# Performance work log

Hardware: AMD Instinct MI355X
Metric: run time of the kernel (lower is better)

The kernel has to match this reference:

```python
import jax, jax.numpy as jnp
import numpy as np

N, E, B = 100000, 1600000, 64
IN, HID, OUT, ED = 64, 128, 128, 2
K, ALPHA = 16, 0.1
LN_EPS = 1e-5


def setup_inputs() -> dict:
    key = jax.random.key(0)
    ks = jax.random.split(key, 24)
    def gl(k, shape, fan_in):
        return jax.random.uniform(k, shape, jnp.float32, -1.0, 1.0) / np.sqrt(fan_in)
    inp = {
        "x": jax.random.normal(ks[0], (N, IN), jnp.float32),
        "edge_index": jax.random.randint(ks[1], (2, E), 0, N, jnp.int64),
        "batch": jnp.sort(jax.random.randint(ks[2], (N,), 0, B, jnp.int64)),
        "edge_attr": jax.random.normal(ks[3], (E, ED), jnp.float32),
        # conv1: edge lin (ED->IN) + mlp (IN->HID->HID)
        "We1": gl(ks[4], (ED, IN), ED), "be1": jnp.zeros((IN,)),
        "W1a": gl(ks[5], (IN, HID), IN), "b1a": jnp.zeros((HID,)),
        "W1b": gl(ks[6], (HID, HID), HID), "b1b": jnp.zeros((HID,)),
        "g1": jnp.ones((HID,)), "bn1": jnp.zeros((HID,)),
        # conv2: edge lin (ED->HID) + mlp (HID->OUT->OUT)
        "We2": gl(ks[7], (ED, HID), ED), "be2": jnp.zeros((HID,)),
        "W2a": gl(ks[8], (HID, OUT), HID), "b2a": jnp.zeros((OUT,)),
        "W2b": gl(ks[9], (OUT, OUT), OUT), "b2b": jnp.zeros((OUT,)),
        "g2": jnp.ones((OUT,)), "bn2": jnp.zeros((OUT,)),
        # gate nn (OUT -> OUT//2 -> 1)
        "Wg1": gl(ks[10], (OUT, OUT // 2), OUT), "bg1": jnp.zeros((OUT // 2,)),
        "Wg2": gl(ks[11], (OUT // 2, 1), OUT // 2), "bg2": jnp.zeros((1,)),
    }
    return inp


def _gelu(x):
    return jax.nn.gelu(x, approximate=False)


def _layernorm(x, g, b):
    mu = jnp.mean(x, axis=-1, keepdims=True)
    var = jnp.mean(jnp.square(x - mu), axis=-1, keepdims=True)
    return (x - mu) * jax.lax.rsqrt(var + LN_EPS) * g + b


def _gine(x, src, dst, edge_attr, We, be, W1, b1, W2, b2):
    # message: ReLU(x_j + lin(edge_attr)), aggregated by sum at dst; eps=0
    m = jax.nn.relu(x[src] + edge_attr @ We + be)          # [E, d]
    agg = jax.ops.segment_sum(m, dst, num_segments=N)      # [N, d]
    h = x + agg
    return _gelu(h @ W1 + b1) @ W2 + b2


def _appnp(x, src, dst):
    # gcn_norm with self-loops: deg_i = 1 + in-degree
    deg = jax.ops.segment_sum(jnp.ones((E,), x.dtype), dst, num_segments=N) + 1.0
    dis = jax.lax.rsqrt(deg)
    w = dis[src] * dis[dst]            # [E]
    selfw = 1.0 / deg                  # [N]
    def step(i, h):
        prop = jax.ops.segment_sum(w[:, None] * h[src], dst, num_segments=N) \
               + selfw[:, None] * h
        return (1.0 - ALPHA) * prop + ALPHA * x
    return jax.lax.fori_loop(0, K, step, x)


def reference(x, edge_index, batch, edge_attr,
              We1, be1, W1a, b1a, W1b, b1b, g1, bn1,
              We2, be2, W2a, b2a, W2b, b2b, g2, bn2,
              Wg1, bg1, Wg2, bg2):
    src, dst = edge_index[0], edge_index[1]
    h = _gine(x, src, dst, edge_attr, We1, be1, W1a, b1a, W1b, b1b)
    h = _layernorm(_gelu(h), g1, bn1)
    # dropout is identity in eval
    h = _gine(h, src, dst, edge_attr, We2, be2, W2a, b2a, W2b, b2b)
    h = _layernorm(h, g2, bn2)
    h = _appnp(h, src, dst)
    # attentional aggregation: per-graph softmax over gate scores
    gate = (_gelu(h @ Wg1 + bg1) @ Wg2 + bg2)[:, 0]        # [N]
    m = jax.ops.segment_max(gate, batch, num_segments=B)    # [B]
    e = jnp.exp(gate - m[batch])
    s = jax.ops.segment_sum(e, batch, num_segments=B)
    a = e / s[batch]
    g = jax.ops.segment_sum(a[:, None] * h, batch, num_segments=B)  # [B, OUT]
    return h, g
```

## Files before the change

kernel.cpp:

```cpp
#include <hip/hip_runtime.h>
#include <math.h>

#define N_NODES 100000
#define N_EDGES 1600000
#define N_B 64
#define D_IN 64
#define D_HID 128
#define D_OUT 128
#define K_ITER 16
#define LN_EPS 1e-5f

#define BSH 9
#define NBUCK 196
#define NBUCK_PAD 200
#define BSPLIT 4
#define CHUNK 2048

typedef short s8v __attribute__((ext_vector_type(8)));
typedef float f4v __attribute__((ext_vector_type(4)));

__device__ __forceinline__ float gelu_f(float x) {
    return 0.5f * x * (1.0f + erff(0.70710678118654752440f * x));
}

__device__ __forceinline__ float ubx(unsigned u) { return __uint_as_float(u << 16); }
__device__ __forceinline__ float uby(unsigned u) { return __uint_as_float(u & 0xffff0000u); }

__device__ __forceinline__ unsigned short bf_rne(float x) {
    unsigned u = __float_as_uint(x);
    u += 0x7fffu + ((u >> 16) & 1u);
    return (unsigned short)(u >> 16);
}
__device__ __forceinline__ float bf_f(unsigned short s) {
    return __uint_as_float(((unsigned)s) << 16);
}
__device__ __forceinline__ unsigned pack_bf2(float a, float b) {
    return (unsigned)bf_rne(a) | (((unsigned)bf_rne(b)) << 16);
}


__global__ __launch_bounds__(256) void hist_kernel(const int* __restrict__ dst, int* __restrict__ counts) {
    int e = blockIdx.x * 256 + threadIdx.x;
    if (e < N_EDGES) atomicAdd(&counts[dst[e]], 1);
}

__global__ __launch_bounds__(256) void deg_kernel(const int* __restrict__ counts,
                                                  float* __restrict__ dis, float* __restrict__ selfw,
                                                  float* __restrict__ rsq) {
    int i = blockIdx.x * 256 + threadIdx.x;
    if (i < N_NODES) {
        float d = (float)(counts[i] + 1);
        dis[i] = 1.0f / sqrtf(d);
        selfw[i] = 1.0f / d;
        rsq[i] = sqrtf(d);
    }
}

__global__ __launch_bounds__(1024) void scan1(const int* __restrict__ counts, int* __restrict__ rp,
                                              int* __restrict__ bsum) {
    __shared__ int tmp[1024];
    int t = threadIdx.x;
    int idx = blockIdx.x * 1024 + t;
    int v = (idx < N_NODES) ? counts[idx] : 0;
    tmp[t] = v;
    __syncthreads();
    for (int o = 1; o < 1024; o <<= 1) {
        int add = (t >= o) ? tmp[t - o] : 0;
        __syncthreads();
        tmp[t] += add;
        __syncthreads();
    }
    if (idx < N_NODES) rp[idx] = tmp[t] - v;
    if (t == 1023) bsum[blockIdx.x] = tmp[t];
}

__global__ void scan2(int* bsum, int nb) {
    if (threadIdx.x == 0 && blockIdx.x == 0) {
        int acc = 0;
        for (int i = 0; i < nb; i++) { int v = bsum[i]; bsum[i] = acc; acc += v; }
    }
}

__global__ __launch_bounds__(1024) void scan3(int* __restrict__ rp, const int* __restrict__ bsum,
                                              int* __restrict__ cursor) {
    int t = threadIdx.x;
    int idx = blockIdx.x * 1024 + t;
    if (idx < N_NODES) {
        int v = rp[idx] + bsum[blockIdx.x];
        rp[idx] = v;
        cursor[idx] = v;
    }
    if (idx == 0) rp[N_NODES] = N_EDGES;
}

__global__ void binit(const int* __restrict__ rp, int* __restrict__ bcursor) {
    int b = threadIdx.x;
    if (b < NBUCK) bcursor[b] = rp[b << BSH];
}

__global__ __launch_bounds__(256) void bin_kernel(const int* __restrict__ src, const int* __restrict__ dst,
                                                  const float* __restrict__ ea,
                                                  int* __restrict__ bcursor, int4* __restrict__ tmp) {
    __shared__ int hist[NBUCK];
    __shared__ int loff[NBUCK];
    __shared__ int gbase[NBUCK];
    __shared__ int total_s;
    __shared__ int4 stage[CHUNK];
    int tid = threadIdx.x;
    int base = blockIdx.x * CHUNK;
    for (int t = tid; t < NBUCK; t += 256) hist[t] = 0;
    __syncthreads();
    int4 rec[8];
    int bk[8], rk[8];
    bool val[8];
    #pragma unroll
    for (int k = 0; k < 8; k++) {
        int e = base + k * 256 + tid;
        val[k] = (e < N_EDGES);
        if (val[k]) {
            int s = src[e], d = dst[e];
            float2 e2 = ((const float2*)ea)[e];
            rec[k].x = s;
            rec[k].y = __float_as_int(e2.x);
            rec[k].z = __float_as_int(e2.y);
            rec[k].w = d;
            bk[k] = d >> BSH;
            rk[k] = atomicAdd(&hist[bk[k]], 1);
        }
    }
    __syncthreads();
    if (tid == 0) {
        int acc = 0;
        for (int b = 0; b < NBUCK; b++) { loff[b] = acc; acc += hist[b]; }
        total_s = acc;
    }
    __syncthreads();
    if (tid < NBUCK && hist[tid] > 0) gbase[tid] = atomicAdd(&bcursor[tid], hist[tid]);
    __syncthreads();
    #pragma unroll
    for (int k = 0; k < 8; k++)
        if (val[k]) stage[loff[bk[k]] + rk[k]] = rec[k];
    __syncthreads();
    int total = total_s;
    for (int s = tid; s < total; s += 256) {
        int lo = 0, hi = NBUCK - 1;
        while (lo < hi) {
            int mid = (lo + hi + 1) >> 1;
            if (loff[mid] <= s) lo = mid; else hi = mid - 1;
        }
        tmp[gbase[lo] + (s - loff[lo])] = stage[s];
    }
}

__global__ __launch_bounds__(256) void scatter2_kernel(const int4* __restrict__ tmp, const int* __restrict__ rp,
                                                       int* __restrict__ cursor, int4* __restrict__ edata) {
    int b = blockIdx.x % NBUCK_PAD;
    int slice = blockIdx.x / NBUCK_PAD;
    if (b >= NBUCK) return;
    int lo = rp[b << BSH];
    int nend = (b + 1) << BSH;
    if (nend > N_NODES) nend = N_NODES;
    int hi = rp[nend];
    for (int i = lo + slice * 256 + threadIdx.x; i < hi; i += BSPLIT * 256) {
        int4 r = tmp[i];
        int pos = atomicAdd(&cursor[r.w], 1);
        edata[pos] = r;
    }
}

__global__ __launch_bounds__(256) void split_kernel(const int4* __restrict__ edata, int* __restrict__ esrc) {
    int e = blockIdx.x * 256 + threadIdx.x;
    if (e < N_EDGES) esrc[e] = edata[e].x;
}

__global__ __launch_bounds__(256) void x_to_bf(const float4* __restrict__ x4, uint2* __restrict__ xb2) {
    int i = blockIdx.x * 256 + threadIdx.x;
    if (i < N_NODES * 16) {
        float4 v = x4[i];
        uint2 o;
        o.x = pack_bf2(v.x, v.y);
        o.y = pack_bf2(v.z, v.w);
        xb2[i] = o;
    }
}


__global__ __launch_bounds__(256) void conv1_gather(const float* __restrict__ x,
                                                    const unsigned short* __restrict__ xb,
                                                    const int* __restrict__ rp,
                                                    const int4* __restrict__ edata,
                                                    const float* __restrict__ We1, const float* __restrict__ be1,
                                                    float* __restrict__ out) {
    int gw = (blockIdx.x * 256 + threadIdx.x) >> 6;
    if (gw >= N_NODES) return;
    int lane = threadIdx.x & 63;
    float w0 = We1[lane], w1 = We1[64 + lane], bb = be1[lane];
    float acc = x[(size_t)gw * 64 + lane];
    int j = rp[gw], jend = rp[gw + 1];
    for (; j + 8 <= jend; j += 8) {
        int4 e0 = edata[j], e1 = edata[j + 1], e2 = edata[j + 2], e3 = edata[j + 3];
        int4 e4 = edata[j + 4], e5 = edata[j + 5], e6 = edata[j + 6], e7 = edata[j + 7];
        unsigned short v0 = xb[(size_t)e0.x * 64 + lane];
        unsigned short v1 = xb[(size_t)e1.x * 64 + lane];
        unsigned short v2 = xb[(size_t)e2.x * 64 + lane];
        unsigned short v3 = xb[(size_t)e3.x * 64 + lane];
        unsigned short v4 = xb[(size_t)e4.x * 64 + lane];
        unsigned short v5 = xb[(size_t)e5.x * 64 + lane];
        unsigned short v6 = xb[(size_t)e6.x * 64 + lane];
        unsigned short v7 = xb[(size_t)e7.x * 64 + lane];
        acc += fmaxf(bf_f(v0) + __int_as_float(e0.y) * w0 + __int_as_float(e0.z) * w1 + bb, 0.0f);
        acc += fmaxf(bf_f(v1) + __int_as_float(e1.y) * w0 + __int_as_float(e1.z) * w1 + bb, 0.0f);
        acc += fmaxf(bf_f(v2) + __int_as_float(e2.y) * w0 + __int_as_float(e2.z) * w1 + bb, 0.0f);
        acc += fmaxf(bf_f(v3) + __int_as_float(e3.y) * w0 + __int_as_float(e3.z) * w1 + bb, 0.0f);
        acc += fmaxf(bf_f(v4) + __int_as_float(e4.y) * w0 + __int_as_float(e4.z) * w1 + bb, 0.0f);
        acc += fmaxf(bf_f(v5) + __int_as_float(e5.y) * w0 + __int_as_float(e5.z) * w1 + bb, 0.0f);
        acc += fmaxf(bf_f(v6) + __int_as_float(e6.y) * w0 + __int_as_float(e6.z) * w1 + bb, 0.0f);
        acc += fmaxf(bf_f(v7) + __int_as_float(e7.y) * w0 + __int_as_float(e7.z) * w1 + bb, 0.0f);
    }
    for (; j < jend; j++) {
        int4 e = edata[j];
        unsigned short v = xb[(size_t)e.x * 64 + lane];
        acc += fmaxf(bf_f(v) + __int_as_float(e.y) * w0 + __int_as_float(e.z) * w1 + bb, 0.0f);
    }
    out[(size_t)gw * 64 + lane] = acc;
}

__global__ __launch_bounds__(256) void conv2_gather(const float* __restrict__ h1f, const unsigned* __restrict__ h1b,
                                                    const int* __restrict__ rp,
                                                    const int4* __restrict__ edata,
                                                    const float* __restrict__ We2, const float* __restrict__ be2,
                                                    float* __restrict__ out) {
    int gw = (blockIdx.x * 256 + threadIdx.x) >> 6;
    if (gw >= N_NODES) return;
    int lane = threadIdx.x & 63;
    int f0 = lane * 2;
    float w00 = We2[f0], w01 = We2[f0 + 1];
    float w10 = We2[128 + f0], w11 = We2[128 + f0 + 1];
    float b0 = be2[f0], b1 = be2[f0 + 1];
    float2 hc = ((const float2*)h1f)[(size_t)gw * 64 + lane];
    float a0 = hc.x, a1 = hc.y;
    int j = rp[gw], jend = rp[gw + 1];
    for (; j + 8 <= jend; j += 8) {
        int4 e0 = edata[j], e1 = edata[j + 1], e2 = edata[j + 2], e3 = edata[j + 3];
        int4 e4 = edata[j + 4], e5 = edata[j + 5], e6 = edata[j + 6], e7 = edata[j + 7];
        unsigned v0 = h1b[(size_t)e0.x * 64 + lane];
        unsigned v1 = h1b[(size_t)e1.x * 64 + lane];
        unsigned v2 = h1b[(size_t)e2.x * 64 + lane];
        unsigned v3 = h1b[(size_t)e3.x * 64 + lane];
        unsigned v4 = h1b[(size_t)e4.x * 64 + lane];
        unsigned v5 = h1b[(size_t)e5.x * 64 + lane];
        unsigned v6 = h1b[(size_t)e6.x * 64 + lane];
        unsigned v7 = h1b[(size_t)e7.x * 64 + lane];
        a0 += fmaxf(ubx(v0) + __int_as_float(e0.y) * w00 + __int_as_float(e0.z) * w10 + b0, 0.0f);
        a1 += fmaxf(uby(v0) + __int_as_float(e0.y) * w01 + __int_as_float(e0.z) * w11 + b1, 0.0f);
        a0 += fmaxf(ubx(v1) + __int_as_float(e1.y) * w00 + __int_as_float(e1.z) * w10 + b0, 0.0f);
        a1 += fmaxf(uby(v1) + __int_as_float(e1.y) * w01 + __int_as_float(e1.z) * w11 + b1, 0.0f);
        a0 += fmaxf(ubx(v2) + __int_as_float(e2.y) * w00 + __int_as_float(e2.z) * w10 + b0, 0.0f);
        a1 += fmaxf(uby(v2) + __int_as_float(e2.y) * w01 + __int_as_float(e2.z) * w11 + b1, 0.0f);
        a0 += fmaxf(ubx(v3) + __int_as_float(e3.y) * w00 + __int_as_float(e3.z) * w10 + b0, 0.0f);
        a1 += fmaxf(uby(v3) + __int_as_float(e3.y) * w01 + __int_as_float(e3.z) * w11 + b1, 0.0f);
        a0 += fmaxf(ubx(v4) + __int_as_float(e4.y) * w00 + __int_as_float(e4.z) * w10 + b0, 0.0f);
        a1 += fmaxf(uby(v4) + __int_as_float(e4.y) * w01 + __int_as_float(e4.z) * w11 + b1, 0.0f);
        a0 += fmaxf(ubx(v5) + __int_as_float(e5.y) * w00 + __int_as_float(e5.z) * w10 + b0, 0.0f);
        a1 += fmaxf(uby(v5) + __int_as_float(e5.y) * w01 + __int_as_float(e5.z) * w11 + b1, 0.0f);
        a0 += fmaxf(ubx(v6) + __int_as_float(e6.y) * w00 + __int_as_float(e6.z) * w10 + b0, 0.0f);
        a1 += fmaxf(uby(v6) + __int_as_float(e6.y) * w01 + __int_as_float(e6.z) * w11 + b1, 0.0f);
        a0 += fmaxf(ubx(v7) + __int_as_float(e7.y) * w00 + __int_as_float(e7.z) * w10 + b0, 0.0f);
        a1 += fmaxf(uby(v7) + __int_as_float(e7.y) * w01 + __int_as_float(e7.z) * w11 + b1, 0.0f);
    }
    for (; j < jend; j++) {
        int4 e = edata[j];
        unsigned v = h1b[(size_t)e.x * 64 + lane];
        a0 += fmaxf(ubx(v) + __int_as_float(e.y) * w00 + __int_as_float(e.z) * w10 + b0, 0.0f);
        a1 += fmaxf(uby(v) + __int_as_float(e.y) * w01 + __int_as_float(e.z) * w11 + b1, 0.0f);
    }
    out[(size_t)gw * 128 + f0] = a0;
    out[(size_t)gw * 128 + f0 + 1] = a1;
}


template <int Kd, bool GELU, bool LN, int OMODE, bool SCALE>
__global__ __launch_bounds__(256) void mlp_mfma(const float* __restrict__ A, const float* __restrict__ W,
                                                const float* __restrict__ bias, const float* __restrict__ g,
                                                const float* __restrict__ bn, float* __restrict__ outf,
                                                unsigned short* __restrict__ outb,
                                                const float* __restrict__ uscale) {
    __shared__ unsigned short sHi[8192];
    __shared__ unsigned short sLo[8192];
    int wave = threadIdx.x >> 6, lane = threadIdx.x & 63;
    int quad = lane >> 4, n = lane & 15;
    int rowA = blockIdx.x * 64 + wave * 16 + n;
    int rowAc = (rowA < N_NODES) ? rowA : 0;

    f4v acc[8];
    #pragma unroll
    for (int t = 0; t < 8; t++) acc[t] = (f4v){0.f, 0.f, 0.f, 0.f};

    for (int ph = 0; ph < Kd / 64; ph++) {
        __syncthreads();
        for (int idx = threadIdx.x; idx < 8192; idx += 256) {
            int k = idx >> 7, c = idx & 127;
            float v = W[(size_t)(ph * 64 + k) * 128 + c];
            unsigned short hi = bf_rne(v);
            unsigned short lo = bf_rne(v - bf_f(hi));
            int kk = k >> 5, q = (k >> 3) & 3, j = k & 7, t = c >> 4, nn = c & 15;
            int lidx = ((((kk * 4 + q) * 8 + t) * 16 + nn) << 3) + j;
            sHi[lidx] = hi;
            sLo[lidx] = lo;
        }
        __syncthreads();
        #pragma unroll
        for (int kk = 0; kk < 2; kk++) {
            int k0 = ph * 64 + kk * 32 + quad * 8;
            const float4* ap = (const float4*)(A + (size_t)rowAc * Kd + k0);
            float4 a0 = ap[0], a1 = ap[1];
            float av[8] = {a0.x, a0.y, a0.z, a0.w, a1.x, a1.y, a1.z, a1.w};
            s8v ahi, alo;
            #pragma unroll
            for (int j = 0; j < 8; j++) {
                unsigned short h = bf_rne(av[j]);
                ahi[j] = (short)h;
                alo[j] = (short)bf_rne(av[j] - bf_f(h));
            }
            int base = ((kk * 4 + quad) * 8) * 128;
            #pragma unroll
            for (int t = 0; t < 8; t++) {
                s8v bhi = *(const s8v*)&sHi[base + ((t * 16 + n) << 3)];
                s8v blo = *(const s8v*)&sLo[base + ((t * 16 + n) << 3)];
                acc[t] = __builtin_amdgcn_mfma_f32_16x16x32_bf16(ahi, bhi, acc[t], 0, 0, 0);
                acc[t] = __builtin_amdgcn_mfma_f32_16x16x32_bf16(ahi, blo, acc[t], 0, 0, 0);
                acc[t] = __builtin_amdgcn_mfma_f32_16x16x32_bf16(alo, bhi, acc[t], 0, 0, 0);
            }
        }
    }

    float bcol[8], gcol[8], bncol[8];
    #pragma unroll
    for (int t = 0; t < 8; t++) {
        bcol[t] = bias[t * 16 + n];
        if (LN) { gcol[t] = g[t * 16 + n]; bncol[t] = bn[t * 16 + n]; }
    }
    #pragma unroll
    for (int r = 0; r < 4; r++) {
        int row = blockIdx.x * 64 + wave * 16 + quad * 4 + r;
        float v[8];
        #pragma unroll
        for (int t = 0; t < 8; t++) {
            float x = acc[t][r] + bcol[t];
            v[t] = GELU ? gelu_f(x) : x;
        }
        if (LN) {
            float s = 0.f, q2 = 0.f;
            #pragma unroll
            for (int t = 0; t < 8; t++) { s += v[t]; q2 += v[t] * v[t]; }
            #pragma unroll
            for (int m = 1; m <= 8; m <<= 1) {
                s += __shfl_xor(s, m, 64);
                q2 += __shfl_xor(q2, m, 64);
            }
            float mu = s * (1.0f / 128.0f);
            float rs = rsqrtf(q2 * (1.0f / 128.0f) - mu * mu + LN_EPS);
            #pragma unroll
            for (int t = 0; t < 8; t++) v[t] = (v[t] - mu) * rs * gcol[t] + bncol[t];
        }
        if (row < N_NODES) {
            float us = SCALE ? uscale[row] : 1.0f;
            #pragma unroll
            for (int t = 0; t < 8; t++) {
                if (OMODE != 2) outf[(size_t)row * 128 + t * 16 + n] = v[t];
                if (OMODE >= 1) outb[(size_t)row * 128 + t * 16 + n] = bf_rne(SCALE ? v[t] * us : v[t]);
            }
        }
    }
}


__global__ __launch_bounds__(256) void gate_mfma(const float* __restrict__ h, const float* __restrict__ Wg1,
                                                 const float* __restrict__ bg1, const float* __restrict__ Wg2,
                                                 const float* __restrict__ bg2, float* __restrict__ gate) {
    __shared__ unsigned short sHi[8192];
    __shared__ unsigned short sLo[8192];
    int wave = threadIdx.x >> 6, lane = threadIdx.x & 63;
    int quad = lane >> 4, n = lane & 15;
    for (int idx = threadIdx.x; idx < 8192; idx += 256) {
        int k = idx >> 6, c = idx & 63;
        float v = Wg1[k * 64 + c];
        unsigned short hi = bf_rne(v);
        unsigned short lo = bf_rne(v - bf_f(hi));
        int kk = k >> 5, q = (k >> 3) & 3, j = k & 7, t = c >> 4, nn = c & 15;
        int lidx = ((((kk * 4 + q) * 4 + t) * 16 + nn) << 3) + j;
        sHi[lidx] = hi;
        sLo[lidx] = lo;
    }
    __syncthreads();
    int rowA = blockIdx.x * 64 + wave * 16 + n;
    int rowAc = (rowA < N_NODES) ? rowA : 0;
    f4v acc[4];
    #pragma unroll
    for (int t = 0; t < 4; t++) acc[t] = (f4v){0.f, 0.f, 0.f, 0.f};
    #pragma unroll
    for (int kk = 0; kk < 4; kk++) {
        const float4* ap = (const float4*)(h + (size_t)rowAc * 128 + kk * 32 + quad * 8);
        float4 a0 = ap[0], a1 = ap[1];
        float av[8] = {a0.x, a0.y, a0.z, a0.w, a1.x, a1.y, a1.z, a1.w};
        s8v ahi, alo;
        #pragma unroll
        for (int j = 0; j < 8; j++) {
            unsigned short hh = bf_rne(av[j]);
            ahi[j] = (short)hh;
            alo[j] = (short)bf_rne(av[j] - bf_f(hh));
        }
        int base = ((kk * 4 + quad) * 4) * 128;
        #pragma unroll
        for (int t = 0; t < 4; t++) {
            s8v bhi = *(const s8v*)&sHi[base + ((t * 16 + n) << 3)];
            s8v blo = *(const s8v*)&sLo[base + ((t * 16 + n) << 3)];
            acc[t] = __builtin_amdgcn_mfma_f32_16x16x32_bf16(ahi, bhi, acc[t], 0, 0, 0);
            acc[t] = __builtin_amdgcn_mfma_f32_16x16x32_bf16(ahi, blo, acc[t], 0, 0, 0);
            acc[t] = __builtin_amdgcn_mfma_f32_16x16x32_bf16(alo, bhi, acc[t], 0, 0, 0);
        }
    }
    float b2 = bg2[0];
    float bb[4], vv[4];
    #pragma unroll
    for (int t = 0; t < 4; t++) { bb[t] = bg1[t * 16 + n]; vv[t] = Wg2[t * 16 + n]; }
    #pragma unroll
    for (int r = 0; r < 4; r++) {
        int row = blockIdx.x * 64 + wave * 16 + quad * 4 + r;
        float val = 0.f;
        #pragma unroll
        for (int t = 0; t < 4; t++) val += gelu_f(acc[t][r] + bb[t]) * vv[t];
        #pragma unroll
        for (int m = 1; m <= 8; m <<= 1) val += __shfl_xor(val, m, 64);
        if (n == 0 && row < N_NODES) gate[row] = val + b2;
    }
}


template <bool LAST>
__global__ __launch_bounds__(256) void appnp_step_u(const unsigned* __restrict__ hin,
                                                    const unsigned* __restrict__ anchor,
                                                    unsigned* __restrict__ hout, float2* __restrict__ houtf,
                                                    const int* __restrict__ rp, const int* __restrict__ esrc,
                                                    const float* __restrict__ selfw,
                                                    const float* __restrict__ rsq) {
    int gw = (blockIdx.x * 256 + threadIdx.x) >> 6;
    if (gw >= N_NODES) return;
    int lane = threadIdx.x & 63;
    size_t idx = (size_t)gw * 64 + lane;
    unsigned hcp = hin[idx];
    float ax = ubx(hcp), ay = uby(hcp);
    int j = rp[gw], jend = rp[gw + 1];
    for (; j + 8 <= jend; j += 8) {
        int s0 = esrc[j],     s1 = esrc[j + 1], s2 = esrc[j + 2], s3 = esrc[j + 3];
        int s4 = esrc[j + 4], s5 = esrc[j + 5], s6 = esrc[j + 6], s7 = esrc[j + 7];
        unsigned v0 = hin[(size_t)s0 * 64 + lane];
        unsigned v1 = hin[(size_t)s1 * 64 + lane];
        unsigned v2 = hin[(size_t)s2 * 64 + lane];
        unsigned v3 = hin[(size_t)s3 * 64 + lane];
        unsigned v4 = hin[(size_t)s4 * 64 + lane];
        unsigned v5 = hin[(size_t)s5 * 64 + lane];
        unsigned v6 = hin[(size_t)s6 * 64 + lane];
        unsigned v7 = hin[(size_t)s7 * 64 + lane];
        ax += ubx(v0); ay += uby(v0);
        ax += ubx(v1); ay += uby(v1);
        ax += ubx(v2); ay += uby(v2);
        ax += ubx(v3); ay += uby(v3);
        ax += ubx(v4); ay += uby(v4);
        ax += ubx(v5); ay += uby(v5);
        ax += ubx(v6); ay += uby(v6);
        ax += ubx(v7); ay += uby(v7);
    }
    for (; j + 4 <= jend; j += 4) {
        int s0 = esrc[j], s1 = esrc[j + 1], s2 = esrc[j + 2], s3 = esrc[j + 3];
        unsigned v0 = hin[(size_t)s0 * 64 + lane];
        unsigned v1 = hin[(size_t)s1 * 64 + lane];
        unsigned v2 = hin[(size_t)s2 * 64 + lane];
        unsigned v3 = hin[(size_t)s3 * 64 + lane];
        ax += ubx(v0); ay += uby(v0);
        ax += ubx(v1); ay += uby(v1);
        ax += ubx(v2); ay += uby(v2);
        ax += ubx(v3); ay += uby(v3);
    }
    for (; j < jend; j++) {
        int s = esrc[j];
        unsigned v = hin[(size_t)s * 64 + lane];
        ax += ubx(v); ay += uby(v);
    }
    float swi = 0.9f * selfw[gw];
    unsigned ancp = anchor[idx];
    float ox = fmaf(swi, ax, 0.1f * ubx(ancp));
    float oy = fmaf(swi, ay, 0.1f * uby(ancp));
    if (LAST) {
        float rq = rsq[gw];
        float2 o; o.x = ox * rq; o.y = oy * rq;
        houtf[idx] = o;
    } else {
        hout[idx] = pack_bf2(ox, oy);
    }
}


__global__ void seg_begin(const int* __restrict__ batch, int* __restrict__ gbeg) {
    int b = threadIdx.x;
    if (b > N_B) return;
    if (b == N_B) { gbeg[N_B] = N_NODES; return; }
    int lo = 0, hi = N_NODES;
    while (lo < hi) {
        int mid = (lo + hi) >> 1;
        if (batch[mid] < b) lo = mid + 1; else hi = mid;
    }
    gbeg[b] = lo;
}

__global__ __launch_bounds__(256) void seg_max(const float* __restrict__ gate, const int* __restrict__ gbeg,
                                               float* __restrict__ gmax) {
    int b = blockIdx.x;
    int s = gbeg[b], e = gbeg[b + 1];
    float m = -INFINITY;
    for (int i = s + threadIdx.x; i < e; i += 256) m = fmaxf(m, gate[i]);
    for (int o = 32; o > 0; o >>= 1) m = fmaxf(m, __shfl_xor(m, o, 64));
    __shared__ float red[4];
    if ((threadIdx.x & 63) == 0) red[threadIdx.x >> 6] = m;
    __syncthreads();
    if (threadIdx.x == 0) gmax[b] = fmaxf(fmaxf(red[0], red[1]), fmaxf(red[2], red[3]));
}

__global__ __launch_bounds__(256) void seg_sum(const float* __restrict__ gate, const int* __restrict__ gbeg,
                                               const float* __restrict__ gmax, float* __restrict__ gsum) {
    int b = blockIdx.x;
    int s = gbeg[b], e = gbeg[b + 1];
    float m = gmax[b];
    float acc = 0.0f;
    for (int i = s + threadIdx.x; i < e; i += 256) acc += expf(gate[i] - m);
    for (int o = 32; o > 0; o >>= 1) acc += __shfl_xor(acc, o, 64);
    __shared__ float red[4];
    if ((threadIdx.x & 63) == 0) red[threadIdx.x >> 6] = acc;
    __syncthreads();
    if (threadIdx.x == 0) gsum[b] = red[0] + red[1] + red[2] + red[3];
}

__global__ __launch_bounds__(512) void seg_pool(const float* __restrict__ h, const float* __restrict__ gate,
                                                const int* __restrict__ gbeg, const float* __restrict__ gmax,
                                                const float* __restrict__ gsum, float* __restrict__ gout) {
    int b = blockIdx.x >> 3, slice = blockIdx.x & 7;
    int team = threadIdx.x >> 7;
    int f = threadIdx.x & 127;
    int s = gbeg[b], e = gbeg[b + 1];
    float m = gmax[b];
    float inv = (e > s) ? 1.0f / gsum[b] : 0.0f;
    float acc = 0.0f;
    for (int i = s + slice * 4 + team; i < e; i += 32) {
        float a = expf(gate[i] - m) * inv;
        acc = fmaf(a, h[(size_t)i * 128 + f], acc);
    }
    __shared__ float red[4][128];
    red[team][f] = acc;
    __syncthreads();
    if (team == 0) {
        float v = red[0][f] + red[1][f] + red[2][f] + red[3][f];
        atomicAdd(&gout[b * 128 + f], v);
    }
}


extern "C" void kernel_launch(void* const* d_in, const int* in_sizes, int n_in,
                              void* d_out, int out_size, void* d_ws, size_t ws_size,
                              hipStream_t stream) {
    const float* x     = (const float*)d_in[0];
    const int*   ei    = (const int*)d_in[1];
    const int*   batch = (const int*)d_in[2];
    const float* ea    = (const float*)d_in[3];
    const float* We1 = (const float*)d_in[4];
    const float* be1 = (const float*)d_in[5];
    const float* W1a = (const float*)d_in[6];
    const float* b1a = (const float*)d_in[7];
    const float* W1b = (const float*)d_in[8];
    const float* b1b = (const float*)d_in[9];
    const float* g1  = (const float*)d_in[10];
    const float* bn1 = (const float*)d_in[11];
    const float* We2 = (const float*)d_in[12];
    const float* be2 = (const float*)d_in[13];
    const float* W2a = (const float*)d_in[14];
    const float* b2a = (const float*)d_in[15];
    const float* W2b = (const float*)d_in[16];
    const float* b2b = (const float*)d_in[17];
    const float* g2  = (const float*)d_in[18];
    const float* bn2 = (const float*)d_in[19];
    const float* Wg1 = (const float*)d_in[20];
    const float* bg1 = (const float*)d_in[21];
    const float* Wg2 = (const float*)d_in[22];
    const float* bg2 = (const float*)d_in[23];

    float* outH = (float*)d_out;
    float* outG = outH + (size_t)N_NODES * 128;

    char* w = (char*)d_ws;
    auto carve = [&](size_t bytes) {
        void* p = (void*)w;
        w += ((bytes + 255) / 256) * 256;
        return p;
    };
    float*  bufB   = (float*)carve((size_t)N_NODES * 128 * 4);
    float*  bufC   = (float*)carve((size_t)N_NODES * 128 * 4);
    int4*   edata  = (int4*)carve((size_t)N_EDGES * 16);
    int*    counts = (int*)carve((size_t)N_NODES * 4);
    int*    rp     = (int*)carve((size_t)(N_NODES + 1) * 4);
    int*    cursor = (int*)carve((size_t)N_NODES * 4);
    float*  dis    = (float*)carve((size_t)N_NODES * 4);
    float*  selfw  = (float*)carve((size_t)N_NODES * 4);
    float*  rsq    = (float*)carve((size_t)N_NODES * 4);
    float*  gate   = (float*)carve((size_t)N_NODES * 4);
    int*    bsum   = (int*)carve(128 * 4);
    int*    bcursor= (int*)carve(NBUCK_PAD * 4);
    float*  gmax   = (float*)carve(N_B * 4);
    float*  gsum   = (float*)carve(N_B * 4);
    int*    gbeg   = (int*)carve((N_B + 1) * 4);

    const int* src = ei;
    const int* dst = ei + N_EDGES;

    const int NB_SCAN = (N_NODES + 1023) / 1024;
    const int EB = (N_EDGES + 255) / 256;
    const int NBLK = (N_NODES + 255) / 256;
    const int WBLK = (N_NODES + 3) / 4;
    const int MBLK = (N_NODES + 63) / 64;
    const int ABLK = (N_EDGES + CHUNK - 1) / CHUNK;

    unsigned short* h1bf  = (unsigned short*)bufC;
    unsigned* ancU  = (unsigned*)bufC;
    unsigned* pingA = ancU + (size_t)N_NODES * 64;
    unsigned* pingB = (unsigned*)bufB;
    unsigned short* xb = (unsigned short*)pingA;
    int*      esrc  = (int*)(bufB + (size_t)N_NODES * 64);
    int4*     tmp   = (int4*)bufB;

    hipMemsetAsync(counts, 0, (size_t)N_NODES * 4, stream);
    hist_kernel<<<EB, 256, 0, stream>>>(dst, counts);
    deg_kernel<<<NBLK, 256, 0, stream>>>(counts, dis, selfw, rsq);
    scan1<<<NB_SCAN, 1024, 0, stream>>>(counts, rp, bsum);
    scan2<<<1, 64, 0, stream>>>(bsum, NB_SCAN);
    scan3<<<NB_SCAN, 1024, 0, stream>>>(rp, bsum, cursor);
    binit<<<1, 256, 0, stream>>>(rp, bcursor);
    bin_kernel<<<ABLK, 256, 0, stream>>>(src, dst, ea, bcursor, tmp);
    scatter2_kernel<<<NBUCK_PAD * BSPLIT, 256, 0, stream>>>(tmp, rp, cursor, edata);
    x_to_bf<<<(N_NODES * 16 + 255) / 256, 256, 0, stream>>>((const float4*)x, (uint2*)xb);

    conv1_gather<<<WBLK, 256, 0, stream>>>(x, xb, rp, edata, We1, be1, bufB);
    mlp_mfma<64, true, false, 0, false><<<MBLK, 256, 0, stream>>>(bufB, W1a, b1a, nullptr, nullptr, outH, nullptr, nullptr);
    mlp_mfma<128, true, true, 1, false><<<MBLK, 256, 0, stream>>>(outH, W1b, b1b, g1, bn1, bufB, h1bf, nullptr);

    conv2_gather<<<WBLK, 256, 0, stream>>>(bufB, (const unsigned*)h1bf, rp, edata, We2, be2, outH);
    mlp_mfma<128, true, false, 0, false><<<MBLK, 256, 0, stream>>>(outH, W2a, b2a, nullptr, nullptr, bufB, nullptr, nullptr);
    mlp_mfma<128, false, true, 2, true><<<MBLK, 256, 0, stream>>>(bufB, W2b, b2b, g2, bn2, nullptr, (unsigned short*)ancU, dis);

    split_kernel<<<EB, 256, 0, stream>>>(edata, esrc);

    const unsigned* cur = ancU;
    for (int k = 1; k <= K_ITER - 1; k++) {
        unsigned* dstbuf = (k & 1) ? pingA : pingB;
        appnp_step_u<false><<<WBLK, 256, 0, stream>>>(cur, ancU, dstbuf, nullptr, rp, esrc, selfw, nullptr);
        cur = dstbuf;
    }
    appnp_step_u<true><<<WBLK, 256, 0, stream>>>(cur, ancU, nullptr, (float2*)outH, rp, esrc, selfw, rsq);

    gate_mfma<<<MBLK, 256, 0, stream>>>(outH, Wg1, bg1, Wg2, bg2, gate);
    seg_begin<<<1, 128, 0, stream>>>(batch, gbeg);
    seg_max<<<N_B, 256, 0, stream>>>(gate, gbeg, gmax);
    seg_sum<<<N_B, 256, 0, stream>>>(gate, gbeg, gmax, gsum);
    hipMemsetAsync(outG, 0, (size_t)N_B * 128 * 4, stream);
    seg_pool<<<N_B * 8, 512, 0, stream>>>(outH, gate, gbeg, gmax, gsum, outG);
}
```

Measured before the change: 1.754 ms.

## Slice APPNP features into 8 feature-major tables to shrink the gather working set

The bf16 node features used by APPNP are stored as 8 separate slices of 16 features each, laid out feature-slice-major. Each propagation kernel handles one slice per block, and a wave covers 8 edges at a time with 8 lanes per edge, finishing with a shuffle reduction across edges. Each slice table is 1/8 the size of the full table, so the random gathers should hit cache more often. The cost is 8x more blocks, repeated reads of the index arrays for every slice, smaller 32-byte gather segments, and only 8 of 64 lanes writing results.

Measured after the change: 5.025 ms. 187% more time.

```diff
diff --git a/kernel.cpp b/kernel.cpp
--- a/kernel.cpp
+++ b/kernel.cpp
@@ -15,6 +15,9 @@
 #define NBUCK_PAD 200
 #define BSPLIT 4
 #define CHUNK 2048
+
+#define NSLICE 8
+#define SLICE_DW 8
 
 typedef short s8v __attribute__((ext_vector_type(8)));
 typedef float f4v __attribute__((ext_vector_type(4)));
@@ -97,6 +100,7 @@
     int b = threadIdx.x;
     if (b < NBUCK) bcursor[b] = rp[b << BSH];
 }
+
 
 __global__ __launch_bounds__(256) void bin_kernel(const int* __restrict__ src, const int* __restrict__ dst,
                                                   const float* __restrict__ ea,
@@ -368,7 +372,11 @@
             #pragma unroll
             for (int t = 0; t < 8; t++) {
                 if (OMODE != 2) outf[(size_t)row * 128 + t * 16 + n] = v[t];
-                if (OMODE >= 1) outb[(size_t)row * 128 + t * 16 + n] = bf_rne(SCALE ? v[t] * us : v[t]);
+                if (OMODE == 1) outb[(size_t)row * 128 + t * 16 + n] = bf_rne(v[t]);
+                if (OMODE == 2) {
+                    outb[(size_t)t * (N_NODES * 16) + (size_t)row * 16 + n] =
+                        bf_rne(SCALE ? v[t] * us : v[t]);
+                }
             }
         }
     }
@@ -438,65 +446,61 @@
 
 
 template <bool LAST>
-__global__ __launch_bounds__(256) void appnp_step_u(const unsigned* __restrict__ hin,
-                                                    const unsigned* __restrict__ anchor,
-                                                    unsigned* __restrict__ hout, float2* __restrict__ houtf,
-                                                    const int* __restrict__ rp, const int* __restrict__ esrc,
-                                                    const float* __restrict__ selfw,
-                                                    const float* __restrict__ rsq) {
-    int gw = (blockIdx.x * 256 + threadIdx.x) >> 6;
-    if (gw >= N_NODES) return;
+__global__ __launch_bounds__(256) void appnp_slice(const unsigned* __restrict__ uin,
+                                                   const unsigned* __restrict__ anc,
+                                                   unsigned* __restrict__ uout, float* __restrict__ houtf,
+                                                   const int* __restrict__ rp, const int* __restrict__ esrc,
+                                                   const float* __restrict__ selfw,
+                                                   const float* __restrict__ rsq) {
+    int slice = blockIdx.x & 7;
+    int node = ((blockIdx.x >> 3) << 2) + (threadIdx.x >> 6);
+    if (node >= N_NODES) return;
     int lane = threadIdx.x & 63;
-    size_t idx = (size_t)gw * 64 + lane;
-    unsigned hcp = hin[idx];
-    float ax = ubx(hcp), ay = uby(hcp);
-    int j = rp[gw], jend = rp[gw + 1];
-    for (; j + 8 <= jend; j += 8) {
-        int s0 = esrc[j],     s1 = esrc[j + 1], s2 = esrc[j + 2], s3 = esrc[j + 3];
-        int s4 = esrc[j + 4], s5 = esrc[j + 5], s6 = esrc[j + 6], s7 = esrc[j + 7];
-        unsigned v0 = hin[(size_t)s0 * 64 + lane];
-        unsigned v1 = hin[(size_t)s1 * 64 + lane];
-        unsigned v2 = hin[(size_t)s2 * 64 + lane];
-        unsigned v3 = hin[(size_t)s3 * 64 + lane];
-        unsigned v4 = hin[(size_t)s4 * 64 + lane];
-        unsigned v5 = hin[(size_t)s5 * 64 + lane];
-        unsigned v6 = hin[(size_t)s6 * 64 + lane];
-        unsigned v7 = hin[(size_t)s7 * 64 + lane];
+    int g = lane >> 3;
+    int fd = lane & 7;
+    const unsigned* tbl = uin + (size_t)slice * ((size_t)N_NODES * SLICE_DW);
+    float ax = 0.f, ay = 0.f;
+    int j = rp[node], jend = rp[node + 1];
+    for (; j + 16 <= jend; j += 16) {
+        int s0 = __builtin_nontemporal_load(esrc + j + g);
+        int s1 = __builtin_nontemporal_load(esrc + j + 8 + g);
+        unsigned v0 = tbl[(size_t)s0 * SLICE_DW + fd];
+        unsigned v1 = tbl[(size_t)s1 * SLICE_DW + fd];
         ax += ubx(v0); ay += uby(v0);
         ax += ubx(v1); ay += uby(v1);
-        ax += ubx(v2); ay += uby(v2);
-        ax += ubx(v3); ay += uby(v3);
-        ax += ubx(v4); ay += uby(v4);
-        ax += ubx(v5); ay += uby(v5);
-        ax += ubx(v6); ay += uby(v6);
-        ax += ubx(v7); ay += uby(v7);
-    }
-    for (; j + 4 <= jend; j += 4) {
-        int s0 = esrc[j], s1 = esrc[j + 1], s2 = esrc[j + 2], s3 = esrc[j + 3];
-        unsigned v0 = hin[(size_t)s0 * 64 + lane];
-        unsigned v1 = hin[(size_t)s1 * 64 + lane];
-        unsigned v2 = hin[(size_t)s2 * 64 + lane];
-        unsigned v3 = hin[(size_t)s3 * 64 + lane];
+    }
+    for (; j + 8 <= jend; j += 8) {
+        int s0 = __builtin_nontemporal_load(esrc + j + g);
+        unsigned v0 = tbl[(size_t)s0 * SLICE_DW + fd];
         ax += ubx(v0); ay += uby(v0);
-        ax += ubx(v1); ay += uby(v1);
-        ax += ubx(v2); ay += uby(v2);
-        ax += ubx(v3); ay += uby(v3);
-    }
-    for (; j < jend; j++) {
-        int s = esrc[j];
-        unsigned v = hin[(size_t)s * 64 + lane];
-        ax += ubx(v); ay += uby(v);
-    }
-    float swi = 0.9f * selfw[gw];
-    unsigned ancp = anchor[idx];
-    float ox = fmaf(swi, ax, 0.1f * ubx(ancp));
-    float oy = fmaf(swi, ay, 0.1f * uby(ancp));
+    }
+    int rem = jend - j;
+    if (g < rem) {
+        int s0 = __builtin_nontemporal_load(esrc + j + g);
+        unsigned v0 = tbl[(size_t)s0 * SLICE_DW + fd];
+        ax += ubx(v0); ay += uby(v0);
+    }
+    ax += __shfl_xor(ax, 8, 64);  ay += __shfl_xor(ay, 8, 64);
+    ax += __shfl_xor(ax, 16, 64); ay += __shfl_xor(ay, 16, 64);
+    ax += __shfl_xor(ax, 32, 64); ay += __shfl_xor(ay, 32, 64);
+    unsigned hc = tbl[(size_t)node * SLICE_DW + fd];
+    ax += ubx(hc); ay += uby(hc);
+    unsigned an = __builtin_nontemporal_load(
+        anc + (size_t)slice * ((size_t)N_NODES * SLICE_DW) + (size_t)node * SLICE_DW + fd);
+    float swi = 0.9f * selfw[node];
+    float ox = fmaf(swi, ax, 0.1f * ubx(an));
+    float oy = fmaf(swi, ay, 0.1f * uby(an));
     if (LAST) {
-        float rq = rsq[gw];
-        float2 o; o.x = ox * rq; o.y = oy * rq;
-        houtf[idx] = o;
+        if (g == 0) {
+            float rq = rsq[node];
+            float2 o; o.x = ox * rq; o.y = oy * rq;
+            ((float2*)houtf)[(size_t)node * 64 + slice * 8 + fd] = o;
+        }
     } else {
-        hout[idx] = pack_bf2(ox, oy);
+        if (g == 0) {
+            uout[(size_t)slice * ((size_t)N_NODES * SLICE_DW) + (size_t)node * SLICE_DW + fd] =
+                pack_bf2(ox, oy);
+        }
     }
 }
 
@@ -626,6 +630,7 @@
     const int WBLK = (N_NODES + 3) / 4;
     const int MBLK = (N_NODES + 63) / 64;
     const int ABLK = (N_EDGES + CHUNK - 1) / CHUNK;
+    const int SBLK = NSLICE * ((N_NODES + 3) / 4);
 
     unsigned short* h1bf  = (unsigned short*)bufC;
     unsigned* ancU  = (unsigned*)bufC;
@@ -659,10 +664,10 @@
     const unsigned* cur = ancU;
     for (int k = 1; k <= K_ITER - 1; k++) {
         unsigned* dstbuf = (k & 1) ? pingA : pingB;
-        appnp_step_u<false><<<WBLK, 256, 0, stream>>>(cur, ancU, dstbuf, nullptr, rp, esrc, selfw, nullptr);
+        appnp_slice<false><<<SBLK, 256, 0, stream>>>(cur, ancU, dstbuf, nullptr, rp, esrc, selfw, nullptr);
         cur = dstbuf;
     }
-    appnp_step_u<true><<<WBLK, 256, 0, stream>>>(cur, ancU, nullptr, (float2*)outH, rp, esrc, selfw, rsq);
+    appnp_slice<true><<<SBLK, 256, 0, stream>>>(cur, ancU, nullptr, outH, rp, esrc, selfw, rsq);
 
     gate_mfma<<<MBLK, 256, 0, stream>>>(outH, Wg1, bg1, Wg2, bg2, gate);
     seg_begin<<<1, 128, 0, stream>>>(batch, gbeg);
```
